# Optimization experiments

Hardware: AMD Instinct MI355X
Metric: run time of the kernel (lower is better)

Reference implementation:

```python
import jax, jax.numpy as jnp
import numpy as np
from jax import lax

N = 50000      # total nodes
E = 400000     # total edges
F = 512        # input feature dim
B = 50         # graphs in batch
NP = 1000      # nodes per graph
OUT = 10       # out_channel
EPS = 1e-5


def setup_inputs():
    key = jax.random.key(0)
    ks = jax.random.split(key, 20)
    x = jax.random.normal(ks[0], (N, F), jnp.float32)
    eg = jnp.arange(E) // (E // B)                       # graph id per edge
    src = jax.random.randint(ks[1], (E,), 0, NP) + eg * NP
    dst = jax.random.randint(ks[2], (E,), 0, NP) + eg * NP
    edge_index = jnp.stack([src, dst]).astype(jnp.int32)
    batch = (jnp.arange(N) // NP).astype(jnp.int32)
    s = 0.02
    W1 = s * jax.random.normal(ks[3], (1024, F), jnp.float32)
    b1 = jnp.zeros((1024,), jnp.float32)
    g1 = jnp.ones((1024,), jnp.float32)
    be1 = jnp.zeros((1024,), jnp.float32)
    Wp = s * jax.random.normal(ks[4], (1, 2 * 1024), jnp.float32)  # EdgePooling lin
    bp = jnp.zeros((1,), jnp.float32)
    W2 = s * jax.random.normal(ks[5], (512, 1024), jnp.float32)
    b2 = jnp.zeros((512,), jnp.float32)
    g2 = jnp.ones((512,), jnp.float32)
    be2 = jnp.zeros((512,), jnp.float32)
    Wfc = s * jax.random.normal(ks[6], (200, 512), jnp.float32)
    bfc = jnp.zeros((200,), jnp.float32)
    Wfc1 = s * jax.random.normal(ks[7], (OUT, 200), jnp.float32)
    bfc1 = jnp.zeros((OUT,), jnp.float32)
    return dict(x=x, edge_index=edge_index, batch=batch, W1=W1, b1=b1, g1=g1,
                be1=be1, Wp=Wp, bp=bp, W2=W2, b2=b2, g2=g2, be2=be2,
                Wfc=Wfc, bfc=bfc, Wfc1=Wfc1, bfc1=bfc1)


def _bn(h, g, b):
    m = h.mean(0)
    v = jnp.var(h, axis=0)  # biased var, as torch BatchNorm1d (train mode)
    return (h - m) * (g / jnp.sqrt(v + EPS)) + b


def _edge_pool(h, src, dst, batch, Wp, bp):
    # raw edge score: Linear([h_src || h_dst]) -> scalar per edge
    e = jnp.concatenate([h[src], h[dst]], axis=-1) @ Wp.T + bp  # [E,1]
    e = e[:, 0]
    # softmax over edges sharing the same destination node (PyG default)
    m = jax.ops.segment_max(e, dst, num_segments=N)
    ex = jnp.exp(e - m[dst])
    den = jax.ops.segment_sum(ex, dst, num_segments=N)
    score = ex / den[dst] + 0.5  # add_to_edge_score = 0.5

    # greedy contraction in descending-score order (sequential, like PyG)
    order = jnp.argsort(-score)
    so, do = src[order], dst[order]

    def step(merged, sd):
        s_, d_ = sd
        ok = (~merged[s_]) & (~merged[d_])
        merged = merged.at[s_].set(merged[s_] | ok)
        merged = merged.at[d_].set(merged[d_] | ok)
        return merged, ok

    _, valid = lax.scan(step, jnp.zeros(N, bool), (so, do))
    ec = (jnp.cumsum(valid.astype(jnp.int32)) - 1)      # cluster id per contracted edge
    num_merged = valid.astype(jnp.int32).sum()

    OOB = jnp.int32(N)
    cluster = jnp.full((N,), -1, jnp.int32)
    cluster = cluster.at[jnp.where(valid, so, OOB)].set(ec, mode='drop')
    cluster = cluster.at[jnp.where(valid, do, OOB)].set(ec, mode='drop')
    unmerged = cluster < 0
    rank = jnp.cumsum(unmerged.astype(jnp.int32)) - 1
    cluster = jnp.where(unmerged, num_merged + rank, cluster)

    # per-cluster multiplier: contracted-edge score, 1.0 for singleton nodes
    mult = jnp.ones((N,), h.dtype)
    mult = mult.at[jnp.where(valid, ec, OOB)].set(score[order], mode='drop')

    new_x = jax.ops.segment_sum(h, cluster, num_segments=N) * mult[:, None]
    new_batch = jnp.full((N,), B, jnp.int32).at[cluster].set(batch)  # pad slots -> dummy graph B
    return new_x, new_batch


def reference(x, edge_index, batch, W1, b1, g1, be1, Wp, bp, W2, b2, g2, be2,
              Wfc, bfc, Wfc1, bfc1):
    src, dst = edge_index[0], edge_index[1]
    # ChebConv K=1 == plain linear (only T_0 = x term)
    h = jax.nn.relu(_bn(x @ W1.T + b1, g1, be1))         # [N,1024]
    h, nb = _edge_pool(h, src, dst, batch, Wp, bp)       # [N,1024] padded, [N]
    h = jax.nn.relu(_bn(h @ W2.T + b2, g2, be2))         # [N,512]
    # global mean pool over graphs (dummy segment B holds padding)
    sums = jax.ops.segment_sum(h, nb, num_segments=B + 1)[:B]
    cnt = jax.ops.segment_sum(jnp.ones((N,), h.dtype), nb, num_segments=B + 1)[:B]
    pooled = sums / jnp.maximum(cnt, 1.0)[:, None]       # [B,512]
    hid = jax.nn.relu(pooled @ Wfc.T + bfc)              # [B,200]; dropout is eval no-op
    return hid @ Wfc1.T + bfc1                           # [B,OUT]
```

## Files before the change

### kernel.cpp

```cpp
#include <hip/hip_runtime.h>

#define Nn   50000
#define Ee   400000
#define Ff   512
#define H1   1024
#define H2   512
#define Bb   50
#define OUTd 10
#define EPSc 1e-5f
#define NPg  1000
#define EPg  8000

typedef _Float16 h8 __attribute__((ext_vector_type(8)));
typedef _Float16 h4 __attribute__((ext_vector_type(4)));
typedef float f4 __attribute__((ext_vector_type(4)));

__device__ __forceinline__ unsigned fmap(float f) {
    unsigned u = __float_as_uint(f);
    return (u & 0x80000000u) ? ~u : (u | 0x80000000u);
}
__device__ __forceinline__ float funmap(unsigned m) {
    unsigned u = (m & 0x80000000u) ? (m ^ 0x80000000u) : ~m;
    return __uint_as_float(u);
}

__device__ __forceinline__ void gl_lds16(const void* g, void* l) {
    __builtin_amdgcn_global_load_lds(
        (const __attribute__((address_space(1))) unsigned int*)g,
        (__attribute__((address_space(3))) unsigned int*)l,
        16, 0, 0);
}

__global__ void init_kernel(double* cs1, double* css1, double* cs2, double* css2, int* scal) {
    int i = blockIdx.x * blockDim.x + threadIdx.x;
    int nth = gridDim.x * blockDim.x;
    for (int j = i; j < H1; j += nth) { cs1[j] = 0.0; css1[j] = 0.0; }
    for (int j = i; j < H2; j += nth) { cs2[j] = 0.0; css2[j] = 0.0; }
    if (i < 16) scal[i] = 0;
}

__global__ void prep_kernel(const float* __restrict__ x, _Float16* __restrict__ xhi, _Float16* __restrict__ xlo,
                            const float* __restrict__ W1, _Float16* __restrict__ w1h, _Float16* __restrict__ w1l,
                            const float* __restrict__ W2, _Float16* __restrict__ w2h) {
    int i = blockIdx.x * blockDim.x + threadIdx.x;
    int nth = gridDim.x * blockDim.x;
    const int nx = Nn * Ff / 4, nw1 = H1 * Ff / 4, nw2 = H2 * H1 / 4;
    for (int k = i; k < nx; k += nth) {
        float4 v = ((const float4*)x)[k];
        h4 H = { (_Float16)v.x, (_Float16)v.y, (_Float16)v.z, (_Float16)v.w };
        h4 L = { (_Float16)(v.x - (float)H[0]), (_Float16)(v.y - (float)H[1]),
                 (_Float16)(v.z - (float)H[2]), (_Float16)(v.w - (float)H[3]) };
        ((h4*)xhi)[k] = H;
        ((h4*)xlo)[k] = L;
    }
    for (int k = i; k < nw1; k += nth) {
        float4 v = ((const float4*)W1)[k];
        h4 H = { (_Float16)v.x, (_Float16)v.y, (_Float16)v.z, (_Float16)v.w };
        h4 L = { (_Float16)(v.x - (float)H[0]), (_Float16)(v.y - (float)H[1]),
                 (_Float16)(v.z - (float)H[2]), (_Float16)(v.w - (float)H[3]) };
        ((h4*)w1h)[k] = H;
        ((h4*)w1l)[k] = L;
    }
    for (int k = i; k < nw2; k += nth) {
        float4 v = ((const float4*)W2)[k];
        h4 H = { (_Float16)v.x, (_Float16)v.y, (_Float16)v.z, (_Float16)v.w };
        ((h4*)w2h)[k] = H;
    }
}

template<int KD, bool SPLIT>
__global__ __launch_bounds__(256) void gemm_mfma_kernel(
        const _Float16* __restrict__ Ahi, const _Float16* __restrict__ Alo,
        const _Float16* __restrict__ Bhi, const _Float16* __restrict__ Blo,
        const float* __restrict__ bias, float* __restrict__ C, int Nc,
        int Mconst, const int* __restrict__ Mptr, int nT,
        double* __restrict__ csum, double* __restrict__ cssum)
{
    const int M = Mptr ? Mptr[0] : Mconst;
    const int nwg = gridDim.x, orig = blockIdx.x;
    const int qq = nwg >> 3, rr = nwg & 7;
    const int xcd = orig & 7, idx = orig >> 3;
    const int lin = (xcd < rr ? xcd * (qq + 1) : rr * (qq + 1) + (xcd - rr) * qq) + idx;
    const int bmI = lin / nT;
    const int bm = bmI * 128, bn = (lin - bmI * nT) * 128;
    if (bm >= M) return;
    constexpr int NARR = SPLIT ? 4 : 2;
    __shared__ __align__(16) _Float16 smem[2][NARR][128 * 32];
    const int tid = threadIdx.x, lane = tid & 63, wave = tid >> 6;
    const int rIn = lane >> 2;
    const int kSrcByte = ((((lane & 3) - ((lane >> 3) & 3)) & 3) << 4);
    const int wr = wave >> 1, wc = wave & 1;
    const int lr = lane & 15, kb = lane >> 4;
    const int pGr = ((kb + ((lr >> 1) & 3)) & 3) << 3;
    f4 acc[4][4] = {};

    auto STAGE = [&](int b, int k0) {
        if (SPLIT) {
            const _Float16* gp = (wave == 0) ? Ahi : (wave == 1) ? Alo : (wave == 2) ? Bhi : Blo;
            _Float16* lp = smem[b][wave];
            const bool isA = (wave < 2);
            const int tb = isA ? bm : bn;
#pragma unroll
            for (int c = 0; c < 8; ++c) {
                int row = tb + c * 16 + rIn;
                if (isA) row = min(row, M - 1);
                gl_lds16((const char*)gp + ((size_t)row * KD + k0) * 2 + kSrcByte, lp + c * 512);
            }
        } else {
            const bool isA = (wave < 2);
            const _Float16* gp = isA ? Ahi : Bhi;
            _Float16* lp = smem[b][isA ? 0 : 1];
            const int tb = isA ? bm : bn;
            const int hf = wave & 1;
#pragma unroll
            for (int c2 = 0; c2 < 4; ++c2) {
                int c = hf * 4 + c2;
                int row = tb + c * 16 + rIn;
                if (isA) row = min(row, M - 1);
                gl_lds16((const char*)gp + ((size_t)row * KD + k0) * 2 + kSrcByte, lp + c * 512);
            }
        }
    };

    int cur = 0;
    STAGE(0, 0);
    for (int k0 = 0; k0 < KD; k0 += 32) {
        __syncthreads();
        if (k0 + 32 < KD) STAGE(cur ^ 1, k0 + 32);
        const _Float16* AhP = smem[cur][0];
        const _Float16* AlP = SPLIT ? smem[cur][1] : nullptr;
        const _Float16* BhP = SPLIT ? smem[cur][2] : smem[cur][1];
        const _Float16* BlP = SPLIT ? smem[cur][3] : nullptr;
        const int ar = (wr * 64 + lr) * 32 + pGr;
        const int br = (wc * 64 + lr) * 32 + pGr;
        h8 ahf[4], bhf[4], alf[4], blf[4];
#pragma unroll
        for (int i = 0; i < 4; ++i) {
            ahf[i] = *(const h8*)&AhP[ar + i * 512];
            bhf[i] = *(const h8*)&BhP[br + i * 512];
            if (SPLIT) {
                alf[i] = *(const h8*)&AlP[ar + i * 512];
                blf[i] = *(const h8*)&BlP[br + i * 512];
            }
        }
#pragma unroll
        for (int mi = 0; mi < 4; ++mi)
#pragma unroll
            for (int ni = 0; ni < 4; ++ni) {
                acc[mi][ni] = __builtin_amdgcn_mfma_f32_16x16x32_f16(ahf[mi], bhf[ni], acc[mi][ni], 0, 0, 0);
                if (SPLIT) {
                    acc[mi][ni] = __builtin_amdgcn_mfma_f32_16x16x32_f16(ahf[mi], blf[ni], acc[mi][ni], 0, 0, 0);
                    acc[mi][ni] = __builtin_amdgcn_mfma_f32_16x16x32_f16(alf[mi], bhf[ni], acc[mi][ni], 0, 0, 0);
                }
            }
        cur ^= 1;
    }
#pragma unroll
    for (int ni = 0; ni < 4; ++ni) {
        const int col = bn + wc * 64 + ni * 16 + lr;
        const float bv = bias[col];
        double sd_ = 0.0, ssd = 0.0;
#pragma unroll
        for (int mi = 0; mi < 4; ++mi)
#pragma unroll
            for (int r = 0; r < 4; ++r) {
                int row = bm + wr * 64 + mi * 16 + kb * 4 + r;
                if (row < M) {
                    float v = acc[mi][ni][r] + bv;
                    C[(size_t)row * Nc + col] = v;
                    sd_ += (double)v;
                    ssd += (double)v * (double)v;
                }
            }
        sd_ += __shfl_xor(sd_, 16); ssd += __shfl_xor(ssd, 16);
        sd_ += __shfl_xor(sd_, 32); ssd += __shfl_xor(ssd, 32);
        if (kb == 0) {
            atomicAdd(&csum[col], sd_);
            atomicAdd(&cssum[col], ssd);
        }
    }
}

__global__ void bnparam_kernel(const double* __restrict__ s, const double* __restrict__ ss,
                               const float* __restrict__ g, const float* __restrict__ be,
                               float* __restrict__ a, float* __restrict__ bb, int cols,
                               const float* __restrict__ padBias, const int* __restrict__ CvPtr) {
    int j = blockIdx.x * blockDim.x + threadIdx.x;
    if (j >= cols) return;
    double sum = s[j], sumsq = ss[j];
    if (CvPtr) {
        double pad = (double)(Nn - CvPtr[0]);
        double bv = padBias ? (double)padBias[j] : 0.0;
        sum += pad * bv; sumsq += pad * bv * bv;
    }
    double mean = sum / (double)Nn;
    double var = sumsq / (double)Nn - mean * mean;
    float aj = g[j] / sqrtf((float)var + EPSc);
    a[j] = aj;
    bb[j] = be[j] - (float)mean * aj;
}

__global__ __launch_bounds__(256) void pq_kernel(const float* __restrict__ h,
        const float* __restrict__ a, const float* __restrict__ bb,
        const float* __restrict__ Wp, float* __restrict__ p, float* __restrict__ q) {
    const int n = blockIdx.x * 4 + (threadIdx.x >> 6);
    if (n >= Nn) return;
    const int lane = threadIdx.x & 63;
    float sp = 0.f, sq = 0.f;
    const float* row = h + (size_t)n * H1;
#pragma unroll
    for (int u = 0; u < 4; ++u) {
        int j = u * 256 + lane * 4;
        float4 v = *(const float4*)(row + j);
        const float4 av = *(const float4*)(a + j);
        const float4 bv = *(const float4*)(bb + j);
        v.x = fmaxf(v.x * av.x + bv.x, 0.f);
        v.y = fmaxf(v.y * av.y + bv.y, 0.f);
        v.z = fmaxf(v.z * av.z + bv.z, 0.f);
        v.w = fmaxf(v.w * av.w + bv.w, 0.f);
        const float4 wp = *(const float4*)(Wp + j);
        const float4 wq = *(const float4*)(Wp + H1 + j);
        sp += v.x * wp.x + v.y * wp.y + v.z * wp.z + v.w * wp.w;
        sq += v.x * wq.x + v.y * wq.y + v.z * wq.z + v.w * wq.w;
    }
#pragma unroll
    for (int off = 32; off > 0; off >>= 1) {
        sp += __shfl_xor(sp, off);
        sq += __shfl_xor(sq, off);
    }
    if (lane == 0) { p[n] = sp; q[n] = sq; }
}

__global__ __launch_bounds__(1024) void match_fused_kernel(
        const int* __restrict__ ei,
        const float* __restrict__ p, const float* __restrict__ q,
        const float* __restrict__ bp,
        unsigned long long* __restrict__ packed,
        int* __restrict__ nodeA, int* __restrict__ nodeB,
        float* __restrict__ multc, int* __restrict__ scal,
        int* __restrict__ gbase, int* __restrict__ gcnt) {
    __shared__ __align__(16) char LB[52096];
    unsigned short* lst = (unsigned short*)LB;
    float* earr = (float*)LB;
    float* pl = (float*)(LB + 32000);
    float* ql = pl + NPg;
    unsigned long long* best = (unsigned long long*)(LB + 32000);
    unsigned* maxu = (unsigned*)(LB + 40000);
    int* mergedS = (int*)(LB + 40000);
    unsigned long long* den = (unsigned long long*)(LB + 44000);
    float* lmult = (float*)(LB + 44000);
    unsigned short* lsA = (unsigned short*)(LB + 48000);
    unsigned short* ldA = (unsigned short*)(LB + 50000);
    int* cnts = (int*)(LB + 52032);

    const int g = blockIdx.x;
    const int tid = threadIdx.x;
    const int e0 = g * EPg, n0 = g * NPg;
    const int* srcp = ei + e0;
    const int* dstp = ei + Ee + e0;
    const float bpv = bp[0];

    for (int i = tid; i < NPg; i += 1024) {
        pl[i] = p[n0 + i];
        ql[i] = q[n0 + i];
        maxu[i] = 0u;
        den[i] = 0ull;
    }
    __syncthreads();
    for (int i = tid; i < EPg; i += 1024) {
        int s = srcp[i] - n0, d = dstp[i] - n0;
        float e = pl[s] + ql[d] + bpv;
        earr[i] = e;
        atomicMax(&maxu[d], fmap(e));
    }
    __syncthreads();
    for (int i = tid; i < EPg; i += 1024) {
        int d = dstp[i] - n0;
        float ex = expf(earr[i] - funmap(maxu[d]));
        atomicAdd(&den[d], (unsigned long long)(ex * 4294967296.0f));
    }
    __syncthreads();
    for (int i = tid; i < EPg; i += 1024) {
        int s = srcp[i] - n0, d = dstp[i] - n0;
        float ex = expf(earr[i] - funmap(maxu[d]));
        float den_f = (float)((double)den[d] * (1.0 / 4294967296.0));
        float sc = ex / den_f + 0.5f;
        packed[e0 + i] = ((unsigned long long)__float_as_uint(sc) << 33)
                       | ((unsigned long long)(8191u - (unsigned)i) << 20)
                       | ((unsigned long long)(unsigned)s << 10) | (unsigned long long)(unsigned)d;
    }
    __syncthreads();
    for (int i = tid; i < NPg; i += 1024) mergedS[i] = 0;
    for (int i = tid; i < EPg; i += 1024) lst[i] = (unsigned short)i;
    if (tid == 0) { cnts[0] = EPg; cnts[1] = 0; cnts[2] = 0; }
    __syncthreads();
    int cur = 0;
    for (int round = 0; round < 20000; ++round) {
        const int n_cur = cnts[cur];
        if (n_cur == 0) break;
        if (tid == 0) cnts[cur ^ 1] = 0;
        for (int i = tid; i < NPg; i += 1024) best[i] = 0ull;
        __syncthreads();
        for (int ii = tid; ii < n_cur; ii += 1024) {
            int le = lst[cur * EPg + ii];
            unsigned long long pk = packed[e0 + le];
            int s = (int)((pk >> 10) & 1023), d = (int)(pk & 1023);
            if (mergedS[s] | mergedS[d]) { lst[cur * EPg + ii] = 0xFFFF; continue; }
            atomicMax(&best[s], pk);
            atomicMax(&best[d], pk);
        }
        __syncthreads();
        for (int ii = tid; ii < n_cur; ii += 1024) {
            int le = lst[cur * EPg + ii];
            if (le == 0xFFFF) continue;
            unsigned long long pk = packed[e0 + le];
            int s = (int)((pk >> 10) & 1023), d = (int)(pk & 1023);
            if (best[s] == pk && best[d] == pk) {
                int c = atomicAdd(&cnts[2], 1);
                lsA[c] = (unsigned short)s;
                ldA[c] = (s == d) ? (unsigned short)0xFFFF : (unsigned short)d;
                lmult[c] = __uint_as_float((unsigned)(pk >> 33));
                mergedS[s] = 1;
                if (d != s) mergedS[d] = 1;
            } else {
                int pos = atomicAdd(&cnts[cur ^ 1], 1);
                lst[(cur ^ 1) * EPg + pos] = (unsigned short)le;
            }
        }
        __syncthreads();
        cur ^= 1;
    }
    for (int i = tid; i < NPg; i += 1024) {
        if (!mergedS[i]) {
            int c = atomicAdd(&cnts[2], 1);
            lsA[c] = (unsigned short)i;
            ldA[c] = 0xFFFF;
            lmult[c] = 1.0f;
        }
    }
    __syncthreads();
    if (tid == 0) {
        int ncl = cnts[2];
        int base = atomicAdd(&scal[2], ncl);
        cnts[3] = base;
        gbase[g] = base;
        gcnt[g] = ncl;
    }
    __syncthreads();
    const int ncl = cnts[2], base = cnts[3];
    for (int i = tid; i < ncl; i += 1024) {
        nodeA[base + i] = n0 + (int)lsA[i];
        nodeB[base + i] = (ldA[i] == 0xFFFF) ? -1 : (n0 + (int)ldA[i]);
        multc[base + i] = lmult[i];
    }
}

__global__ __launch_bounds__(256) void gather_kernel(const float* __restrict__ h,
        const float* __restrict__ a, const float* __restrict__ bb,
        const int* __restrict__ nodeA, const int* __restrict__ nodeB,
        const float* __restrict__ multc, const int* __restrict__ scal,
        _Float16* __restrict__ Ag) {
    int c = blockIdx.x * 4 + (threadIdx.x >> 6);
    if (c >= scal[2]) return;
    const int lane = threadIdx.x & 63;
    int na = nodeA[c], nb = nodeB[c];
    float mu = multc[c];
#pragma unroll
    for (int u = 0; u < 4; ++u) {
        int j = u * 256 + lane * 4;
        const float4 av = *(const float4*)(a + j);
        const float4 bv = *(const float4*)(bb + j);
        float4 v = *(const float4*)(h + (size_t)na * H1 + j);
        v.x = fmaxf(v.x * av.x + bv.x, 0.f);
        v.y = fmaxf(v.y * av.y + bv.y, 0.f);
        v.z = fmaxf(v.z * av.z + bv.z, 0.f);
        v.w = fmaxf(v.w * av.w + bv.w, 0.f);
        if (nb >= 0) {
            float4 w = *(const float4*)(h + (size_t)nb * H1 + j);
            v.x += fmaxf(w.x * av.x + bv.x, 0.f);
            v.y += fmaxf(w.y * av.y + bv.y, 0.f);
            v.z += fmaxf(w.z * av.z + bv.z, 0.f);
            v.w += fmaxf(w.w * av.w + bv.w, 0.f);
        }
        h4 o = { (_Float16)(mu * v.x), (_Float16)(mu * v.y), (_Float16)(mu * v.z), (_Float16)(mu * v.w) };
        *(h4*)(Ag + (size_t)c * H1 + j) = o;
    }
}

__global__ __launch_bounds__(256) void pool_seg_kernel(const float* __restrict__ C2,
        const float* __restrict__ a2, const float* __restrict__ bb2,
        const int* __restrict__ gbase, const int* __restrict__ gcnt,
        float* __restrict__ pool) {
    const int g = blockIdx.x;
    const int j = blockIdx.y * 256 + threadIdx.x;
    const int b0 = gbase[g], cN = gcnt[g];
    const float aj = a2[j], bj = bb2[j];
    float s = 0.f;
    for (int c = b0; c < b0 + cN; ++c)
        s += fmaxf(C2[(size_t)c * H2 + j] * aj + bj, 0.f);
    pool[g * H2 + j] = s;
}

__global__ void fc1_kernel(const float* __restrict__ pool, const int* __restrict__ gcnt,
                           const float* __restrict__ Wfc, const float* __restrict__ bfc,
                           float* __restrict__ hid) {
    int g = blockIdx.x;
    int o = threadIdx.x;
    float inv = 1.0f / fmaxf((float)gcnt[g], 1.0f);
    if (o < 200) {
        float s = 0.f;
        for (int j = 0; j < H2; ++j) s += (pool[g * H2 + j] * inv) * Wfc[o * H2 + j];
        hid[g * 200 + o] = fmaxf(s + bfc[o], 0.f);
    }
}
__global__ void fc2_kernel(const float* __restrict__ hid, const float* __restrict__ Wfc1,
                           const float* __restrict__ bfc1, float* __restrict__ out) {
    int idx = threadIdx.x;
    if (idx < Bb * OUTd) {
        int g = idx / OUTd, o = idx % OUTd;
        float s = bfc1[o];
        for (int t = 0; t < 200; ++t) s += hid[g * 200 + t] * Wfc1[o * 200 + t];
        out[idx] = s;
    }
}

extern "C" void kernel_launch(void* const* d_in, const int* in_sizes, int n_in,
                              void* d_out, int out_size, void* d_ws, size_t ws_size,
                              hipStream_t stream) {
    (void)in_sizes; (void)n_in; (void)out_size; (void)ws_size;
    const float* x    = (const float*)d_in[0];
    const int*   ei   = (const int*)d_in[1];
    const float* W1   = (const float*)d_in[3];
    const float* b1   = (const float*)d_in[4];
    const float* g1   = (const float*)d_in[5];
    const float* be1  = (const float*)d_in[6];
    const float* Wp   = (const float*)d_in[7];
    const float* bp   = (const float*)d_in[8];
    const float* W2   = (const float*)d_in[9];
    const float* b2   = (const float*)d_in[10];
    const float* g2   = (const float*)d_in[11];
    const float* be2  = (const float*)d_in[12];
    const float* Wfc  = (const float*)d_in[13];
    const float* bfc  = (const float*)d_in[14];
    const float* Wfc1 = (const float*)d_in[15];
    const float* bfc1 = (const float*)d_in[16];

    char* w = (char*)d_ws;
    auto take = [&](size_t bytes) -> char* {
        char* r = w;
        w += (bytes + 255) & ~(size_t)255;
        return r;
    };
    float* h      = (float*)take((size_t)Nn * H1 * 4);
    _Float16* xhi = (_Float16*)take((size_t)Nn * Ff * 2);
    _Float16* xlo = (_Float16*)take((size_t)Nn * Ff * 2);
    _Float16* w1h = (_Float16*)take((size_t)H1 * Ff * 2);
    _Float16* w1l = (_Float16*)take((size_t)H1 * Ff * 2);
    _Float16* w2h = (_Float16*)take((size_t)H2 * H1 * 2);
    float* p      = (float*)take((size_t)Nn * 4);
    float* q      = (float*)take((size_t)Nn * 4);
    unsigned long long* packed = (unsigned long long*)take((size_t)Ee * 8);
    int* nodeA    = (int*)take((size_t)Nn * 4);
    int* nodeB    = (int*)take((size_t)Nn * 4);
    float* multc  = (float*)take((size_t)Nn * 4);
    double* cs1   = (double*)take((size_t)H1 * 8);
    double* css1  = (double*)take((size_t)H1 * 8);
    double* cs2   = (double*)take((size_t)H2 * 8);
    double* css2  = (double*)take((size_t)H2 * 8);
    float* a1     = (float*)take((size_t)H1 * 4);
    float* bb1    = (float*)take((size_t)H1 * 4);
    float* a2     = (float*)take((size_t)H2 * 4);
    float* bb2    = (float*)take((size_t)H2 * 4);
    float* pool   = (float*)take((size_t)Bb * H2 * 4);
    float* hid    = (float*)take((size_t)Bb * 200 * 4);
    int* scal     = (int*)take(64 * 4);
    int* gbase    = (int*)take(64 * 4);
    int* gcnt     = (int*)take(64 * 4);
    _Float16* Ag  = xhi;
    float* C2o    = h;

    const int mT = (Nn + 127) / 128;

    init_kernel<<<dim3(16), dim3(256), 0, stream>>>(cs1, css1, cs2, css2, scal);
    prep_kernel<<<dim3(2048), dim3(256), 0, stream>>>(x, xhi, xlo, W1, w1h, w1l, W2, w2h);
    gemm_mfma_kernel<Ff, true><<<dim3(mT * (H1 / 128)), dim3(256), 0, stream>>>(
        xhi, xlo, w1h, w1l, b1, h, H1, Nn, nullptr, H1 / 128, cs1, css1);
    bnparam_kernel<<<dim3((H1 + 255) / 256), dim3(256), 0, stream>>>(cs1, css1, g1, be1, a1, bb1, H1, (const float*)nullptr, (const int*)nullptr);
    pq_kernel<<<dim3((Nn + 3) / 4), dim3(256), 0, stream>>>(h, a1, bb1, Wp, p, q);
    match_fused_kernel<<<dim3(Bb), dim3(1024), 0, stream>>>(ei, p, q, bp, packed,
        nodeA, nodeB, multc, scal, gbase, gcnt);
    gather_kernel<<<dim3((Nn + 3) / 4), dim3(256), 0, stream>>>(h, a1, bb1, nodeA, nodeB, multc, scal, Ag);
    gemm_mfma_kernel<H1, false><<<dim3(mT * (H2 / 128)), dim3(256), 0, stream>>>(
        Ag, nullptr, w2h, nullptr, b2, C2o, H2, 0, scal + 2, H2 / 128, cs2, css2);
    bnparam_kernel<<<dim3((H2 + 255) / 256), dim3(256), 0, stream>>>(cs2, css2, g2, be2, a2, bb2, H2, b2, scal + 2);
    pool_seg_kernel<<<dim3(Bb, H2 / 256), dim3(256), 0, stream>>>(C2o, a2, bb2, gbase, gcnt, pool);
    fc1_kernel<<<dim3(Bb), dim3(256), 0, stream>>>(pool, gcnt, Wfc, bfc, hid);
    fc2_kernel<<<dim3(1), dim3(512), 0, stream>>>(hid, Wfc1, bfc1, (float*)d_out);
}
```

Measured before the change: 702.8 us.

## Use 256x256 tile GEMM with 512 threads for first split-fp16 layer

Adds a dedicated first-layer GEMM kernel with 256x256 output tiles and 8 waves, replacing the generic 128x128 kernel for the x@W1 product. Each wave computes a 128x64 sub-tile using the three-MFMA hi/lo split, with double-buffered LDS staging where each wave loads one of the four operand arrays. Larger tiles raise arithmetic intensity and cut global/L2 traffic per FLOP. The cost is higher register pressure (128 accumulator floats plus fragments), 64KB of LDS and fewer workgroups, which can lower occupancy. The grid also has a ragged last row tile.

```diff
diff --git a/kernel.cpp b/kernel.cpp
--- a/kernel.cpp
+++ b/kernel.cpp
@@ -65,6 +65,100 @@
         float4 v = ((const float4*)W2)[k];
         h4 H = { (_Float16)v.x, (_Float16)v.y, (_Float16)v.z, (_Float16)v.w };
         ((h4*)w2h)[k] = H;
+    }
+}
+
+__global__ __launch_bounds__(512) void gemm1_256_kernel(
+        const _Float16* __restrict__ Ahi, const _Float16* __restrict__ Alo,
+        const _Float16* __restrict__ Bhi, const _Float16* __restrict__ Blo,
+        const float* __restrict__ bias, float* __restrict__ C,
+        double* __restrict__ csum, double* __restrict__ cssum)
+{
+    const int M = Nn;
+    const int nwg = gridDim.x, orig = blockIdx.x;
+    const int qq = nwg >> 3, rr = nwg & 7;
+    const int xcd = orig & 7, idx = orig >> 3;
+    const int lin = (xcd < rr ? xcd * (qq + 1) : rr * (qq + 1) + (xcd - rr) * qq) + idx;
+    const int nT = H1 / 256;
+    const int bmI = lin / nT;
+    const int bm = bmI * 256, bn = (lin - bmI * nT) * 256;
+    __shared__ __align__(16) _Float16 smem[2][4][256 * 32];
+    const int tid = threadIdx.x, lane = tid & 63, wave = tid >> 6;
+    const int rIn = lane >> 2;
+    const int kSrcByte = ((((lane & 3) - ((lane >> 3) & 3)) & 3) << 4);
+    const int wr = wave >> 2, wc = wave & 3;
+    const int lr = lane & 15, kb = lane >> 4;
+    const int pGr = ((kb + ((lr >> 1) & 3)) & 3) << 3;
+    const int arr = wave >> 1;
+    const int hv = wave & 1;
+    const bool isA = (arr < 2);
+    const _Float16* gp = (arr == 0) ? Ahi : (arr == 1) ? Alo : (arr == 2) ? Bhi : Blo;
+    const int tb = isA ? bm : bn;
+    f4 acc[8][4] = {};
+
+    auto STAGE = [&](int b, int k0) {
+        _Float16* lp = smem[b][arr] + hv * (128 * 32);
+#pragma unroll
+        for (int c = 0; c < 8; ++c) {
+            int row = tb + hv * 128 + c * 16 + rIn;
+            if (isA) row = min(row, M - 1);
+            gl_lds16((const char*)gp + ((size_t)row * Ff + k0) * 2 + kSrcByte, lp + c * 512);
+        }
+    };
+
+    int cur = 0;
+    STAGE(0, 0);
+    for (int k0 = 0; k0 < Ff; k0 += 32) {
+        __syncthreads();
+        if (k0 + 32 < Ff) STAGE(cur ^ 1, k0 + 32);
+        const _Float16* AhP = smem[cur][0];
+        const _Float16* AlP = smem[cur][1];
+        const _Float16* BhP = smem[cur][2];
+        const _Float16* BlP = smem[cur][3];
+        h8 ahf[8], alf[8];
+#pragma unroll
+        for (int mi = 0; mi < 8; ++mi) {
+            const int ar = (wr * 128 + mi * 16 + lr) * 32 + pGr;
+            ahf[mi] = *(const h8*)&AhP[ar];
+            alf[mi] = *(const h8*)&AlP[ar];
+        }
+#pragma unroll
+        for (int ni = 0; ni < 4; ++ni) {
+            const int br = (wc * 64 + ni * 16 + lr) * 32 + pGr;
+            const h8 bh = *(const h8*)&BhP[br];
+            const h8 bl = *(const h8*)&BlP[br];
+#pragma unroll
+            for (int mi = 0; mi < 8; ++mi) {
+                acc[mi][ni] = __builtin_amdgcn_mfma_f32_16x16x32_f16(ahf[mi], bh, acc[mi][ni], 0, 0, 0);
+                acc[mi][ni] = __builtin_amdgcn_mfma_f32_16x16x32_f16(ahf[mi], bl, acc[mi][ni], 0, 0, 0);
+                acc[mi][ni] = __builtin_amdgcn_mfma_f32_16x16x32_f16(alf[mi], bh, acc[mi][ni], 0, 0, 0);
+            }
+        }
+        cur ^= 1;
+    }
+#pragma unroll
+    for (int ni = 0; ni < 4; ++ni) {
+        const int col = bn + wc * 64 + ni * 16 + lr;
+        const float bv = bias[col];
+        double sd_ = 0.0, ssd = 0.0;
+#pragma unroll
+        for (int mi = 0; mi < 8; ++mi)
+#pragma unroll
+            for (int r = 0; r < 4; ++r) {
+                int row = bm + wr * 128 + mi * 16 + kb * 4 + r;
+                if (row < M) {
+                    float v = acc[mi][ni][r] + bv;
+                    C[(size_t)row * H1 + col] = v;
+                    sd_ += (double)v;
+                    ssd += (double)v * (double)v;
+                }
+            }
+        sd_ += __shfl_xor(sd_, 16); ssd += __shfl_xor(ssd, 16);
+        sd_ += __shfl_xor(sd_, 32); ssd += __shfl_xor(ssd, 32);
+        if (kb == 0) {
+            atomicAdd(&csum[col], sd_);
+            atomicAdd(&cssum[col], ssd);
+        }
     }
 }
 
@@ -479,12 +573,13 @@
     _Float16* Ag  = xhi;
     float* C2o    = h;
 
-    const int mT = (Nn + 127) / 128;
+    const int mT  = (Nn + 127) / 128;
+    const int mT2 = (Nn + 255) / 256;
 
     init_kernel<<<dim3(16), dim3(256), 0, stream>>>(cs1, css1, cs2, css2, scal);
     prep_kernel<<<dim3(2048), dim3(256), 0, stream>>>(x, xhi, xlo, W1, w1h, w1l, W2, w2h);
-    gemm_mfma_kernel<Ff, true><<<dim3(mT * (H1 / 128)), dim3(256), 0, stream>>>(
-        xhi, xlo, w1h, w1l, b1, h, H1, Nn, nullptr, H1 / 128, cs1, css1);
+    gemm1_256_kernel<<<dim3(mT2 * (H1 / 256)), dim3(512), 0, stream>>>(
+        xhi, xlo, w1h, w1l, b1, h, cs1, css1);
     bnparam_kernel<<<dim3((H1 + 255) / 256), dim3(256), 0, stream>>>(cs1, css1, g1, be1, a1, bb1, H1, (const float*)nullptr, (const int*)nullptr);
     pq_kernel<<<dim3((Nn + 3) / 4), dim3(256), 0, stream>>>(h, a1, bb1, Wp, p, q);
     match_fused_kernel<<<dim3(Bb), dim3(1024), 0, stream>>>(ei, p, q, bp, packed,
```

Result: faster. 674.5 us (-4.0%).
